# Optimization experiments

Measured on AMD Instinct MI355X. Metric: run time of the kernel, lower is better.

The kernel has to match this reference:

```python
import jax, jax.numpy as jnp
import numpy as np

B, L, HID, NH = 4, 1024, 768, 12
HD = HID // NH  # head dim 64
VOCAB, MPE = 30, 2048
NW, WL = 8, 16
BETA = 1.0


def setup_inputs() -> dict:
    key = jax.random.key(0)
    ks = jax.random.split(key, 10)
    hidden_states = jax.random.normal(ks[0], (B, L, HID), dtype=jnp.float32)
    attention_mask = jnp.zeros((B, 1, 1, L), dtype=jnp.float32)
    distance = jax.random.randint(ks[1], (B, L, L), 0, 1022, dtype=jnp.int32)
    random_walk = jax.random.randint(ks[2], (B, L, NW, WL), 0, VOCAB, dtype=jnp.int32)
    anonymous_random_walk = jax.random.randint(ks[3], (B, L, NW, WL), 0, VOCAB, dtype=jnp.int32)
    s = 0.02
    Wq = jax.random.normal(ks[4], (HID, HID), dtype=jnp.float32) * s
    Wk = jax.random.normal(ks[5], (HID, HID), dtype=jnp.float32) * s
    Wv = jax.random.normal(ks[6], (HID, HID), dtype=jnp.float32) * s
    bq = jnp.zeros((HID,), jnp.float32)
    bk = jnp.zeros((HID,), jnp.float32)
    bv = jnp.zeros((HID,), jnp.float32)
    node_emb = jax.random.normal(ks[7], (VOCAB, HID), dtype=jnp.float32) * s
    node_emb = node_emb.at[0].set(0.0)  # padding_idx=0
    dist_emb = jax.random.normal(ks[8], (MPE, NH), dtype=jnp.float32) * s
    dist_emb = dist_emb.at[0].set(0.0)  # padding_idx=0
    return dict(hidden_states=hidden_states, attention_mask=attention_mask,
                Wq=Wq, bq=bq, Wk=Wk, bk=bk, Wv=Wv, bv=bv,
                node_emb=node_emb, dist_emb=dist_emb,
                distance=distance, random_walk=random_walk,
                anonymous_random_walk=anonymous_random_walk)


def _heads(x):  # [B,L,HID] -> [B,NH,L,HD]
    return x.reshape(B, L, NH, HD).transpose(0, 2, 1, 3)


def _walk_bias(walk, node_emb):
    # walk: [B,L,NW,WL] int -> embed [B,L,NW,WL,HID] -> sum dims (2,3) -> [B,L,HID]
    pe = jnp.sum(node_emb[walk], axis=(2, 3))
    e = _heads(pe)  # [B,NH,L,HD]
    return jnp.einsum('bhid,bhjd->bhij', e, e)


def reference(hidden_states, attention_mask, Wq, bq, Wk, bk, Wv, bv,
              node_emb, dist_emb, distance, random_walk, anonymous_random_walk):
    q = _heads(hidden_states @ Wq.T + bq)
    k = _heads(hidden_states @ Wk.T + bk)
    v = _heads(hidden_states @ Wv.T + bv)
    scores = jnp.einsum('bhid,bhjd->bhij', q, k) / np.sqrt(HD).astype(np.float32)
    # distance RPE: [B,L,L,NH] -> [B,NH,L,L]
    bias = dist_emb[distance + 1].transpose(0, 3, 1, 2)
    bias = bias + _walk_bias(random_walk, node_emb)
    bias = bias + _walk_bias(anonymous_random_walk, node_emb)
    scores = scores + bias * BETA + attention_mask
    probs = jax.nn.softmax(scores, axis=-1)
    ctx = jnp.einsum('bhij,bhjd->bhid', probs, v)
    return ctx.transpose(0, 2, 1, 3).reshape(B, L, HID)
```

## Files before the change

### kernel.cpp

```cpp
#include <hip/hip_runtime.h>
#include <hip/hip_bf16.h>

#define LL 1024
#define HID 768
#define NH 12
#define HD 64
#define KAUG 192
#define NBH 48

typedef unsigned int u32;
typedef unsigned short u16;
typedef __bf16 bf16_t;
typedef bf16_t bf16x8 __attribute__((ext_vector_type(8)));
typedef float f32x4 __attribute__((ext_vector_type(4)));
typedef u32 u32x4 __attribute__((ext_vector_type(4)));

__device__ __forceinline__ u16 f2b(float f) {
    union { float f; u32 u; } v; v.f = f;
    u32 r = v.u + 0x7fffu + ((v.u >> 16) & 1u);
    return (u16)(r >> 16);
}
__device__ __forceinline__ bf16x8 load8s(const u16* p) {
    return __builtin_bit_cast(bf16x8, *reinterpret_cast<const u32x4*>(p));
}
__device__ __forceinline__ void cvt4_store_v(u16* dst, float4 f) {
    ushort4 o;
    o.x = f2b(f.x); o.y = f2b(f.y); o.z = f2b(f.z); o.w = f2b(f.w);
    *reinterpret_cast<ushort4*>(dst) = o;
}

__global__ __launch_bounds__(256) void k_qkv(const float* __restrict__ hs,
                                             const float* __restrict__ Wq, const float* __restrict__ Wk,
                                             const float* __restrict__ Wv,
                                             const float* __restrict__ bq, const float* __restrict__ bk,
                                             const float* __restrict__ bv,
                                             u16* __restrict__ Qa, u16* __restrict__ Ka,
                                             u16* __restrict__ Vt) {
    __shared__ __align__(16) u16 smem[18432];
    u16* a_s = smem;
    u16* b_s = smem + 9216;
    int m0 = blockIdx.x * 128;
    int nt = blockIdx.y;
    int which = nt / 6;
    int n0w = (nt % 6) * 128;
    const float* W    = (which == 0) ? Wq : (which == 1) ? Wk : Wv;
    const float* bias = (which == 0) ? bq : (which == 1) ? bk : bv;
    int tid = threadIdx.x;
    int wave = tid >> 6, lane = tid & 63, l15 = lane & 15, qd = lane >> 4;
    int wm = wave >> 1, wn = wave & 1;

    int srow = tid >> 4, scol = (tid & 15) * 4;

    f32x4 acc[4][4];
    for (int i = 0; i < 4; i++)
        for (int j = 0; j < 4; j++) acc[i][j] = f32x4{0.f, 0.f, 0.f, 0.f};

    float4 pa[8], pb[8];
#pragma unroll
    for (int it = 0; it < 8; it++) {
        int row = srow + it * 16;
        pa[it] = *reinterpret_cast<const float4*>(&hs[(size_t)(m0 + row) * 768 + scol]);
        pb[it] = *reinterpret_cast<const float4*>(&W[(size_t)(n0w + row) * 768 + scol]);
    }
    for (int k0 = 0; k0 < 768; k0 += 64) {
        __syncthreads();
#pragma unroll
        for (int it = 0; it < 8; it++) {
            int row = srow + it * 16;
            cvt4_store_v(&a_s[row * 72 + scol], pa[it]);
            cvt4_store_v(&b_s[row * 72 + scol], pb[it]);
        }
        __syncthreads();
        if (k0 < 704) {
            int k1 = k0 + 64;
#pragma unroll
            for (int it = 0; it < 8; it++) {
                int row = srow + it * 16;
                pa[it] = *reinterpret_cast<const float4*>(&hs[(size_t)(m0 + row) * 768 + k1 + scol]);
                pb[it] = *reinterpret_cast<const float4*>(&W[(size_t)(n0w + row) * 768 + k1 + scol]);
            }
        }
        for (int kk = 0; kk < 2; kk++) {
            bf16x8 af[4], bf[4];
            for (int i = 0; i < 4; i++) af[i] = load8s(&a_s[(wm * 64 + i * 16 + l15) * 72 + kk * 32 + qd * 8]);
            for (int j = 0; j < 4; j++) bf[j] = load8s(&b_s[(wn * 64 + j * 16 + l15) * 72 + kk * 32 + qd * 8]);
            for (int i = 0; i < 4; i++)
                for (int j = 0; j < 4; j++)
                    acc[i][j] = __builtin_amdgcn_mfma_f32_16x16x32_bf16(af[i], bf[j], acc[i][j], 0, 0, 0);
        }
    }
    __syncthreads();
    int b = m0 >> 10, l0b = m0 & 1023;
    if (which != 2) {
        float qscale = (which == 0) ? 0.125f : 1.0f;
        for (int i = 0; i < 4; i++) {
            int m_loc = wm * 64 + i * 16 + qd * 4;
            for (int j = 0; j < 4; j++) {
                int n_loc = wn * 64 + j * 16 + l15;
                float bv_ = bias[n0w + n_loc];
                for (int r = 0; r < 4; r++)
                    smem[(m_loc + r) * 136 + n_loc] = f2b((acc[i][j][r] + bv_) * qscale);
            }
        }
        __syncthreads();
        u16* dstbuf = (which == 0) ? Qa : Ka;
        for (int it = 0; it < 8; it++) {
            int c = tid + it * 256;
            int row = c >> 4, col = (c & 15) * 8;
            u32x4 w = *reinterpret_cast<u32x4*>(&smem[row * 136 + col]);
            int nn = n0w + col;
            int h = nn >> 6, d = nn & 63;
            size_t dst = ((size_t)(b * NH + h) * LL + (l0b + row)) * KAUG + d;
            *reinterpret_cast<u32x4*>(&dstbuf[dst]) = w;
        }
    } else {
        for (int i = 0; i < 4; i++) {
            int m_loc = wm * 64 + i * 16 + qd * 4;
            for (int j = 0; j < 4; j++) {
                int n_loc = wn * 64 + j * 16 + l15;
                float bv_ = bias[n0w + n_loc];
                for (int r = 0; r < 4; r++)
                    smem[n_loc * 136 + (m_loc + r)] = f2b(acc[i][j][r] + bv_);
            }
        }
        __syncthreads();
        for (int it = 0; it < 8; it++) {
            int c = tid + it * 256;
            int n = c >> 4, m_off = (c & 15) * 8;
            u32x4 w = *reinterpret_cast<u32x4*>(&smem[n * 136 + m_off]);
            int nn = n0w + n;
            int h = nn >> 6, d = nn & 63;
            size_t dst = ((size_t)(b * NH + h) * HD + d) * LL + (l0b + m_off);
            *reinterpret_cast<u32x4*>(&Vt[dst]) = w;
        }
    }
}

__global__ __launch_bounds__(256) void k_pe(const int* __restrict__ rw,
                                            const int* __restrict__ arw,
                                            const float* __restrict__ node_emb,
                                            u16* __restrict__ Qa, u16* __restrict__ Ka) {
    int m = blockIdx.x;
    __shared__ int hist[64];
    __shared__ float c1[32], c2[32];
    int t = threadIdx.x;
    if (t < 64) hist[t] = 0;
    __syncthreads();
    if (t < 128) atomicAdd(&hist[rw[m * 128 + t] & 31], 1);
    else         atomicAdd(&hist[32 + (arw[m * 128 + (t - 128)] & 31)], 1);
    __syncthreads();
    if (t < 64) {
        if (t < 32) c1[t] = (float)hist[t];
        else        c2[t - 32] = (float)hist[t];
    }
    __syncthreads();
    int b = m >> 10, l = m & 1023;
    for (int c = t; c < 768; c += 256) {
        float s1 = 0.f, s2 = 0.f;
        for (int v = 0; v < 30; v++) {
            float ne = node_emb[v * 768 + c];
            s1 += c1[v] * ne;
            s2 += c2[v] * ne;
        }
        int h = c >> 6, d = c & 63;
        size_t base = ((size_t)(b * NH + h) * LL + l) * KAUG;
        u16 e1 = f2b(s1), e2 = f2b(s2);
        Qa[base + 64 + d] = e1;  Ka[base + 64 + d] = e1;
        Qa[base + 128 + d] = e2; Ka[base + 128 + d] = e2;
    }
}

__global__ __launch_bounds__(256) void k_attn(const u16* __restrict__ Qa, const u16* __restrict__ Ka,
                                              const u16* __restrict__ Vt,
                                              const int* __restrict__ distance,
                                              const float* __restrict__ dist_emb,
                                              const float* __restrict__ mask,
                                              void* __restrict__ outv, int f32mode) {
    __shared__ __align__(16) u16 ka_s[64][200];
    __shared__ __align__(16) u16 vt_s[64][72];
    __shared__ __align__(16) u16 p_s[4][16][72];
    __shared__ float distcol[2048];

    int itile = blockIdx.x;
    int bh = blockIdx.y;
    int b = bh / NH, h = bh % NH;
    int tid = threadIdx.x, wave = tid >> 6, lane = tid & 63, l15 = lane & 15, qd = lane >> 4;

    const u16* Qh = Qa + (size_t)bh * LL * KAUG;
    const u16* Kh = Ka + (size_t)bh * LL * KAUG;
    const u16* Vh = Vt + (size_t)bh * HD * LL;
    const int* distb = distance + (size_t)b * LL * LL;
    const float* maskb = mask + (size_t)b * LL;

    for (int t = tid; t < 2048; t += 256) distcol[t] = dist_emb[t * NH + h];

    int krow = (tid * 6 + 0) / 24;
    (void)krow;

    int i0 = itile * 64 + wave * 16;
    bf16x8 aq[6];
    for (int ks = 0; ks < 6; ks++)
        aq[ks] = load8s(&Qh[(size_t)(i0 + l15) * KAUG + ks * 32 + qd * 8]);

    f32x4 o[4];
    for (int i = 0; i < 4; i++) o[i] = f32x4{0.f, 0.f, 0.f, 0.f};
    float m_i[4], l_i[4];
    for (int r = 0; r < 4; r++) { m_i[r] = -1e30f; l_i[r] = 0.f; }

    u32x4 kbuf[6], vbuf[2];
#pragma unroll
    for (int it = 0; it < 6; it++) {
        int c = tid + it * 256;
        int row = c / 24, col = (c % 24) * 8;
        kbuf[it] = *reinterpret_cast<const u32x4*>(&Kh[(size_t)row * KAUG + col]);
    }
#pragma unroll
    for (int it = 0; it < 2; it++) {
        int c = tid + it * 256;
        int d = c >> 3, col = (c & 7) * 8;
        vbuf[it] = *reinterpret_cast<const u32x4*>(&Vh[(size_t)d * LL + col]);
    }
    int dpre[16]; float mpre[4];
    for (int nf = 0; nf < 4; nf++) {
        int j_abs = nf * 16 + l15;
        mpre[nf] = maskb[j_abs];
        for (int r = 0; r < 4; r++)
            dpre[nf * 4 + r] = distb[(size_t)(i0 + qd * 4 + r) * LL + j_abs];
    }

    for (int jt = 0; jt < 16; jt++) {
        int j0 = jt * 64;
        __syncthreads();
#pragma unroll
        for (int it = 0; it < 6; it++) {
            int c = tid + it * 256;
            int row = c / 24, col = (c % 24) * 8;
            *reinterpret_cast<u32x4*>(&ka_s[row][col]) = kbuf[it];
        }
#pragma unroll
        for (int it = 0; it < 2; it++) {
            int c = tid + it * 256;
            int d = c >> 3, col = (c & 7) * 8;
            *reinterpret_cast<u32x4*>(&vt_s[d][col]) = vbuf[it];
        }
        __syncthreads();
        int dcur[16]; float mcur[4];
        for (int u_ = 0; u_ < 16; u_++) dcur[u_] = dpre[u_];
        for (int u_ = 0; u_ < 4; u_++)  mcur[u_] = mpre[u_];
        if (jt < 15) {
            int j0n = j0 + 64;
#pragma unroll
            for (int it = 0; it < 6; it++) {
                int c = tid + it * 256;
                int row = c / 24, col = (c % 24) * 8;
                kbuf[it] = *reinterpret_cast<const u32x4*>(&Kh[(size_t)(j0n + row) * KAUG + col]);
            }
#pragma unroll
            for (int it = 0; it < 2; it++) {
                int c = tid + it * 256;
                int d = c >> 3, col = (c & 7) * 8;
                vbuf[it] = *reinterpret_cast<const u32x4*>(&Vh[(size_t)d * LL + j0n + col]);
            }
            for (int nf = 0; nf < 4; nf++) {
                int j_abs = j0n + nf * 16 + l15;
                mpre[nf] = maskb[j_abs];
                for (int r = 0; r < 4; r++)
                    dpre[nf * 4 + r] = distb[(size_t)(i0 + qd * 4 + r) * LL + j_abs];
            }
        }

        f32x4 s[4];
        for (int nf = 0; nf < 4; nf++) {
            f32x4 accv = f32x4{0.f, 0.f, 0.f, 0.f};
            for (int ks = 0; ks < 6; ks++) {
                bf16x8 bfrag = load8s(&ka_s[nf * 16 + l15][ks * 32 + qd * 8]);
                accv = __builtin_amdgcn_mfma_f32_16x16x32_bf16(aq[ks], bfrag, accv, 0, 0, 0);
            }
            s[nf] = accv;
        }
        for (int nf = 0; nf < 4; nf++)
            for (int r = 0; r < 4; r++)
                s[nf][r] += distcol[dcur[nf * 4 + r] + 1] + mcur[nf];
        float mx[4];
        for (int r = 0; r < 4; r++) {
            float v = fmaxf(fmaxf(s[0][r], s[1][r]), fmaxf(s[2][r], s[3][r]));
            for (int off = 1; off < 16; off <<= 1) v = fmaxf(v, __shfl_xor(v, off));
            mx[r] = v;
        }
        float alpha[4], rs[4];
        for (int r = 0; r < 4; r++) {
            float mnew = fmaxf(m_i[r], mx[r]);
            alpha[r] = __expf(m_i[r] - mnew);
            m_i[r] = mnew;
            rs[r] = 0.f;
        }
        for (int nf = 0; nf < 4; nf++)
            for (int r = 0; r < 4; r++) {
                float p = __expf(s[nf][r] - m_i[r]);
                rs[r] += p;
                p_s[wave][qd * 4 + r][nf * 16 + l15] = f2b(p);
            }
        for (int r = 0; r < 4; r++) {
            float v = rs[r];
            for (int off = 1; off < 16; off <<= 1) v += __shfl_xor(v, off);
            l_i[r] = l_i[r] * alpha[r] + v;
        }
        for (int df = 0; df < 4; df++)
            for (int r = 0; r < 4; r++) o[df][r] *= alpha[r];
        __builtin_amdgcn_sched_barrier(0);
        asm volatile("" ::: "memory");
        for (int kstep = 0; kstep < 2; kstep++) {
            bf16x8 ap = load8s(&p_s[wave][l15][kstep * 32 + qd * 8]);
            for (int df = 0; df < 4; df++) {
                bf16x8 bv_ = load8s(&vt_s[df * 16 + l15][kstep * 32 + qd * 8]);
                o[df] = __builtin_amdgcn_mfma_f32_16x16x32_bf16(ap, bv_, o[df], 0, 0, 0);
            }
        }
    }
    for (int df = 0; df < 4; df++) {
        int d = df * 16 + l15;
        for (int r = 0; r < 4; r++) {
            int i_abs = i0 + qd * 4 + r;
            float v = o[df][r] / l_i[r];
            size_t idx = ((size_t)(b * LL) + i_abs) * HID + h * 64 + d;
            if (f32mode) ((float*)outv)[idx] = v;
            else         ((u16*)outv)[idx] = f2b(v);
        }
    }
}

extern "C" void kernel_launch(void* const* d_in, const int* in_sizes, int n_in,
                              void* d_out, int out_size, void* d_ws, size_t ws_size,
                              hipStream_t stream) {
    const float* hs       = (const float*)d_in[0];
    const float* mask     = (const float*)d_in[1];
    const float* Wq       = (const float*)d_in[2];
    const float* bq       = (const float*)d_in[3];
    const float* Wk       = (const float*)d_in[4];
    const float* bk       = (const float*)d_in[5];
    const float* Wv       = (const float*)d_in[6];
    const float* bv       = (const float*)d_in[7];
    const float* node_emb = (const float*)d_in[8];
    const float* dist_emb = (const float*)d_in[9];
    const int* distance   = (const int*)d_in[10];
    const int* rw         = (const int*)d_in[11];
    const int* arw        = (const int*)d_in[12];

    int f32mode = 0;
    {
        hipDeviceptr_t base = nullptr; size_t sz = 0;
        if (hipMemGetAddressRange(&base, &sz, (hipDeviceptr_t)d_out) == hipSuccess) {
            size_t off = (size_t)((char*)d_out - (char*)base);
            if (sz - off >= (size_t)out_size * 4u) f32mode = 1;
        }
    }

    u16* Qa = (u16*)d_ws;
    u16* Ka = Qa + (size_t)NBH * LL * KAUG;
    u16* Vt = Ka + (size_t)NBH * LL * KAUG;

    k_qkv<<<dim3(32, 18), dim3(256), 0, stream>>>(hs, Wq, Wk, Wv, bq, bk, bv, Qa, Ka, Vt);
    k_pe<<<dim3(4096), dim3(256), 0, stream>>>(rw, arw, node_emb, Qa, Ka);
    k_attn<<<dim3(16, 48), dim3(256), 0, stream>>>(Qa, Ka, Vt, distance, dist_emb, mask, d_out, f32mode);
}
```

Before: 248.7 us.

## Compute transposed scores to keep P in registers, skip rescale, vectorize loads

Swaps the QK MFMA operands so each lane holds a score column for one query row. That lets the P probabilities feed the PV MFMA (f16 16x16x16) directly from registers, with no LDS staging, and reduces the per-row reductions to two cross-quadrant shuffles. It also adds a lazy softmax rescale that is skipped unless the max grows by more than 8, and stores V as fp16 and the distance table as bf16 in LDS. Distance, mask and PE writes become vectorized, and it adds setprio hints and launch_bounds occupancy 4. The risk is precision loss from fp16 V and P and from the bf16 distance bias.

```diff
diff --git a/kernel.cpp b/kernel.cpp
--- a/kernel.cpp
+++ b/kernel.cpp
@@ -12,6 +12,7 @@
 typedef unsigned short u16;
 typedef __bf16 bf16_t;
 typedef bf16_t bf16x8 __attribute__((ext_vector_type(8)));
+typedef _Float16 f16x4 __attribute__((ext_vector_type(4)));
 typedef float f32x4 __attribute__((ext_vector_type(4)));
 typedef u32 u32x4 __attribute__((ext_vector_type(4)));
 
@@ -20,8 +21,18 @@
     u32 r = v.u + 0x7fffu + ((v.u >> 16) & 1u);
     return (u16)(r >> 16);
 }
+__device__ __forceinline__ float b2f(u16 v) {
+    union { u32 u; float f; } x; x.u = ((u32)v) << 16; return x.f;
+}
+__device__ __forceinline__ u16 f2h(float f) {
+    _Float16 h = (_Float16)f;
+    return __builtin_bit_cast(u16, h);
+}
 __device__ __forceinline__ bf16x8 load8s(const u16* p) {
     return __builtin_bit_cast(bf16x8, *reinterpret_cast<const u32x4*>(p));
+}
+__device__ __forceinline__ f16x4 load4h(const u16* p) {
+    return __builtin_bit_cast(f16x4, *reinterpret_cast<const unsigned long long*>(p));
 }
 __device__ __forceinline__ void cvt4_store_v(u16* dst, float4 f) {
     ushort4 o;
@@ -120,7 +131,7 @@
                 int n_loc = wn * 64 + j * 16 + l15;
                 float bv_ = bias[n0w + n_loc];
                 for (int r = 0; r < 4; r++)
-                    smem[n_loc * 136 + (m_loc + r)] = f2b(acc[i][j][r] + bv_);
+                    smem[n_loc * 136 + (m_loc + r)] = f2h(acc[i][j][r] + bv_);
             }
         }
         __syncthreads();
@@ -143,6 +154,7 @@
     int m = blockIdx.x;
     __shared__ int hist[64];
     __shared__ float c1[32], c2[32];
+    __shared__ __align__(16) u16 pe_s[12 * 128];
     int t = threadIdx.x;
     if (t < 64) hist[t] = 0;
     __syncthreads();
@@ -154,7 +166,6 @@
         else        c2[t - 32] = (float)hist[t];
     }
     __syncthreads();
-    int b = m >> 10, l = m & 1023;
     for (int c = t; c < 768; c += 256) {
         float s1 = 0.f, s2 = 0.f;
         for (int v = 0; v < 30; v++) {
@@ -163,23 +174,29 @@
             s2 += c2[v] * ne;
         }
         int h = c >> 6, d = c & 63;
-        size_t base = ((size_t)(b * NH + h) * LL + l) * KAUG;
-        u16 e1 = f2b(s1), e2 = f2b(s2);
-        Qa[base + 64 + d] = e1;  Ka[base + 64 + d] = e1;
-        Qa[base + 128 + d] = e2; Ka[base + 128 + d] = e2;
-    }
-}
-
-__global__ __launch_bounds__(256) void k_attn(const u16* __restrict__ Qa, const u16* __restrict__ Ka,
-                                              const u16* __restrict__ Vt,
-                                              const int* __restrict__ distance,
-                                              const float* __restrict__ dist_emb,
-                                              const float* __restrict__ mask,
-                                              void* __restrict__ outv, int f32mode) {
+        pe_s[h * 128 + d]      = f2b(s1);
+        pe_s[h * 128 + 64 + d] = f2b(s2);
+    }
+    __syncthreads();
+    int b = m >> 10, l = m & 1023;
+    if (t < 192) {
+        int h = t >> 4, ch = t & 15;
+        u32x4 w = *reinterpret_cast<const u32x4*>(&pe_s[h * 128 + ch * 8]);
+        size_t dst = ((size_t)(b * NH + h) * LL + l) * KAUG + 64 + ch * 8;
+        *reinterpret_cast<u32x4*>(&Qa[dst]) = w;
+        *reinterpret_cast<u32x4*>(&Ka[dst]) = w;
+    }
+}
+
+__global__ __launch_bounds__(256, 4) void k_attn(const u16* __restrict__ Qa, const u16* __restrict__ Ka,
+                                                 const u16* __restrict__ Vt,
+                                                 const int* __restrict__ distance,
+                                                 const float* __restrict__ dist_emb,
+                                                 const float* __restrict__ mask,
+                                                 void* __restrict__ outv, int f32mode) {
     __shared__ __align__(16) u16 ka_s[64][200];
-    __shared__ __align__(16) u16 vt_s[64][72];
-    __shared__ __align__(16) u16 p_s[4][16][72];
-    __shared__ float distcol[2048];
+    __shared__ __align__(16) u16 vt_s[64][80];
+    __shared__ u16 distcol[2048];
 
     int itile = blockIdx.x;
     int bh = blockIdx.y;
@@ -192,22 +209,21 @@
     const int* distb = distance + (size_t)b * LL * LL;
     const float* maskb = mask + (size_t)b * LL;
 
-    for (int t = tid; t < 2048; t += 256) distcol[t] = dist_emb[t * NH + h];
-
-    int krow = (tid * 6 + 0) / 24;
-    (void)krow;
+    for (int t = tid; t < 2048; t += 256) distcol[t] = f2b(dist_emb[t * NH + h]);
 
     int i0 = itile * 64 + wave * 16;
     bf16x8 aq[6];
+#pragma unroll
     for (int ks = 0; ks < 6; ks++)
         aq[ks] = load8s(&Qh[(size_t)(i0 + l15) * KAUG + ks * 32 + qd * 8]);
 
     f32x4 o[4];
+#pragma unroll
     for (int i = 0; i < 4; i++) o[i] = f32x4{0.f, 0.f, 0.f, 0.f};
-    float m_i[4], l_i[4];
-    for (int r = 0; r < 4; r++) { m_i[r] = -1e30f; l_i[r] = 0.f; }
+    float m_i = -1e30f, l_i = 0.f;
 
     u32x4 kbuf[6], vbuf[2];
+    int4 dpre[4];
 #pragma unroll
     for (int it = 0; it < 6; it++) {
         int c = tid + it * 256;
@@ -220,13 +236,9 @@
         int d = c >> 3, col = (c & 7) * 8;
         vbuf[it] = *reinterpret_cast<const u32x4*>(&Vh[(size_t)d * LL + col]);
     }
-    int dpre[16]; float mpre[4];
-    for (int nf = 0; nf < 4; nf++) {
-        int j_abs = nf * 16 + l15;
-        mpre[nf] = maskb[j_abs];
-        for (int r = 0; r < 4; r++)
-            dpre[nf * 4 + r] = distb[(size_t)(i0 + qd * 4 + r) * LL + j_abs];
-    }
+#pragma unroll
+    for (int jf = 0; jf < 4; jf++)
+        dpre[jf] = *reinterpret_cast<const int4*>(&distb[(size_t)(i0 + l15) * LL + jf * 16 + qd * 4]);
 
     for (int jt = 0; jt < 16; jt++) {
         int j0 = jt * 64;
@@ -244,9 +256,6 @@
             *reinterpret_cast<u32x4*>(&vt_s[d][col]) = vbuf[it];
         }
         __syncthreads();
-        int dcur[16]; float mcur[4];
-        for (int u_ = 0; u_ < 16; u_++) dcur[u_] = dpre[u_];
-        for (int u_ = 0; u_ < 4; u_++)  mcur[u_] = mpre[u_];
         if (jt < 15) {
             int j0n = j0 + 64;
 #pragma unroll
@@ -261,70 +270,101 @@
                 int d = c >> 3, col = (c & 7) * 8;
                 vbuf[it] = *reinterpret_cast<const u32x4*>(&Vh[(size_t)d * LL + j0n + col]);
             }
-            for (int nf = 0; nf < 4; nf++) {
-                int j_abs = j0n + nf * 16 + l15;
-                mpre[nf] = maskb[j_abs];
-                for (int r = 0; r < 4; r++)
-                    dpre[nf * 4 + r] = distb[(size_t)(i0 + qd * 4 + r) * LL + j_abs];
-            }
-        }
-
-        f32x4 s[4];
-        for (int nf = 0; nf < 4; nf++) {
-            f32x4 accv = f32x4{0.f, 0.f, 0.f, 0.f};
-            for (int ks = 0; ks < 6; ks++) {
-                bf16x8 bfrag = load8s(&ka_s[nf * 16 + l15][ks * 32 + qd * 8]);
-                accv = __builtin_amdgcn_mfma_f32_16x16x32_bf16(aq[ks], bfrag, accv, 0, 0, 0);
-            }
-            s[nf] = accv;
-        }
-        for (int nf = 0; nf < 4; nf++)
-            for (int r = 0; r < 4; r++)
-                s[nf][r] += distcol[dcur[nf * 4 + r] + 1] + mcur[nf];
-        float mx[4];
-        for (int r = 0; r < 4; r++) {
-            float v = fmaxf(fmaxf(s[0][r], s[1][r]), fmaxf(s[2][r], s[3][r]));
-            for (int off = 1; off < 16; off <<= 1) v = fmaxf(v, __shfl_xor(v, off));
-            mx[r] = v;
-        }
-        float alpha[4], rs[4];
-        for (int r = 0; r < 4; r++) {
-            float mnew = fmaxf(m_i[r], mx[r]);
-            alpha[r] = __expf(m_i[r] - mnew);
-            m_i[r] = mnew;
-            rs[r] = 0.f;
-        }
-        for (int nf = 0; nf < 4; nf++)
-            for (int r = 0; r < 4; r++) {
-                float p = __expf(s[nf][r] - m_i[r]);
-                rs[r] += p;
-                p_s[wave][qd * 4 + r][nf * 16 + l15] = f2b(p);
-            }
-        for (int r = 0; r < 4; r++) {
-            float v = rs[r];
-            for (int off = 1; off < 16; off <<= 1) v += __shfl_xor(v, off);
-            l_i[r] = l_i[r] * alpha[r] + v;
-        }
-        for (int df = 0; df < 4; df++)
-            for (int r = 0; r < 4; r++) o[df][r] *= alpha[r];
-        __builtin_amdgcn_sched_barrier(0);
-        asm volatile("" ::: "memory");
-        for (int kstep = 0; kstep < 2; kstep++) {
-            bf16x8 ap = load8s(&p_s[wave][l15][kstep * 32 + qd * 8]);
+        }
+
+        f32x4 st[4];
+#pragma unroll
+        for (int jf = 0; jf < 4; jf++) st[jf] = f32x4{0.f, 0.f, 0.f, 0.f};
+        __builtin_amdgcn_s_setprio(1);
+#pragma unroll
+        for (int ks = 0; ks < 6; ks++) {
+#pragma unroll
+            for (int jf = 0; jf < 4; jf++) {
+                bf16x8 ak = load8s(&ka_s[jf * 16 + l15][ks * 32 + qd * 8]);
+                st[jf] = __builtin_amdgcn_mfma_f32_16x16x32_bf16(ak, aq[ks], st[jf], 0, 0, 0);
+            }
+        }
+        __builtin_amdgcn_s_setprio(0);
+
+#pragma unroll
+        for (int jf = 0; jf < 4; jf++) {
+            float4 mk = *reinterpret_cast<const float4*>(&maskb[j0 + jf * 16 + qd * 4]);
+            st[jf][0] += b2f(distcol[dpre[jf].x + 1]) + mk.x;
+            st[jf][1] += b2f(distcol[dpre[jf].y + 1]) + mk.y;
+            st[jf][2] += b2f(distcol[dpre[jf].z + 1]) + mk.z;
+            st[jf][3] += b2f(distcol[dpre[jf].w + 1]) + mk.w;
+        }
+        if (jt < 15) {
+            int j0n = j0 + 64;
+#pragma unroll
+            for (int jf = 0; jf < 4; jf++)
+                dpre[jf] = *reinterpret_cast<const int4*>(&distb[(size_t)(i0 + l15) * LL + j0n + jf * 16 + qd * 4]);
+        }
+
+        float m0_ = fmaxf(fmaxf(st[0][0], st[0][1]), fmaxf(st[0][2], st[0][3]));
+        float m1_ = fmaxf(fmaxf(st[1][0], st[1][1]), fmaxf(st[1][2], st[1][3]));
+        float m2_ = fmaxf(fmaxf(st[2][0], st[2][1]), fmaxf(st[2][2], st[2][3]));
+        float m3_ = fmaxf(fmaxf(st[3][0], st[3][1]), fmaxf(st[3][2], st[3][3]));
+        float mx = fmaxf(fmaxf(m0_, m1_), fmaxf(m2_, m3_));
+        mx = fmaxf(mx, __shfl_xor(mx, 16));
+        mx = fmaxf(mx, __shfl_xor(mx, 32));
+        if (!__all(mx <= m_i + 8.0f)) {
+            float mnew = fmaxf(m_i, mx);
+            float alpha = __expf(m_i - mnew);
+            m_i = mnew;
+            l_i *= alpha;
+            float a0 = __shfl(alpha, qd * 4 + 0, 16);
+            float a1 = __shfl(alpha, qd * 4 + 1, 16);
+            float a2 = __shfl(alpha, qd * 4 + 2, 16);
+            float a3 = __shfl(alpha, qd * 4 + 3, 16);
+#pragma unroll
             for (int df = 0; df < 4; df++) {
-                bf16x8 bv_ = load8s(&vt_s[df * 16 + l15][kstep * 32 + qd * 8]);
-                o[df] = __builtin_amdgcn_mfma_f32_16x16x32_bf16(ap, bv_, o[df], 0, 0, 0);
-            }
-        }
-    }
+                o[df][0] *= a0; o[df][1] *= a1; o[df][2] *= a2; o[df][3] *= a3;
+            }
+        }
+        float ssum = 0.f;
+        f16x4 pf[4];
+#pragma unroll
+        for (int jf = 0; jf < 4; jf++) {
+            float p0 = __expf(st[jf][0] - m_i);
+            float p1 = __expf(st[jf][1] - m_i);
+            float p2 = __expf(st[jf][2] - m_i);
+            float p3 = __expf(st[jf][3] - m_i);
+            ssum += (p0 + p1) + (p2 + p3);
+            pf[jf] = f16x4{(_Float16)p0, (_Float16)p1, (_Float16)p2, (_Float16)p3};
+        }
+        ssum += __shfl_xor(ssum, 16);
+        ssum += __shfl_xor(ssum, 32);
+        l_i += ssum;
+
+        __builtin_amdgcn_s_setprio(1);
+#pragma unroll
+        for (int jf = 0; jf < 4; jf++) {
+#pragma unroll
+            for (int df = 0; df < 4; df++) {
+                f16x4 vf = load4h(&vt_s[df * 16 + l15][jf * 16 + qd * 4]);
+                o[df] = __builtin_amdgcn_mfma_f32_16x16x16f16(pf[jf], vf, o[df], 0, 0, 0);
+            }
+        }
+        __builtin_amdgcn_s_setprio(0);
+    }
+
+    float lr0 = 1.f / __shfl(l_i, qd * 4 + 0, 16);
+    float lr1 = 1.f / __shfl(l_i, qd * 4 + 1, 16);
+    float lr2 = 1.f / __shfl(l_i, qd * 4 + 2, 16);
+    float lr3 = 1.f / __shfl(l_i, qd * 4 + 3, 16);
+#pragma unroll
     for (int df = 0; df < 4; df++) {
         int d = df * 16 + l15;
-        for (int r = 0; r < 4; r++) {
-            int i_abs = i0 + qd * 4 + r;
-            float v = o[df][r] / l_i[r];
-            size_t idx = ((size_t)(b * LL) + i_abs) * HID + h * 64 + d;
-            if (f32mode) ((float*)outv)[idx] = v;
-            else         ((u16*)outv)[idx] = f2b(v);
+        float v0 = o[df][0] * lr0, v1 = o[df][1] * lr1, v2 = o[df][2] * lr2, v3 = o[df][3] * lr3;
+        int i_abs = i0 + qd * 4;
+        size_t idx = ((size_t)(b * LL) + i_abs) * HID + h * 64 + d;
+        if (f32mode) {
+            float* op = (float*)outv;
+            op[idx] = v0; op[idx + HID] = v1; op[idx + 2 * HID] = v2; op[idx + 3 * HID] = v3;
+        } else {
+            u16* op = (u16*)outv;
+            op[idx] = f2b(v0); op[idx + HID] = f2b(v1); op[idx + 2 * HID] = f2b(v2); op[idx + 3 * HID] = f2b(v3);
         }
     }
 }
```

Measured after the change: 272.7 us. 9.6% more time.
